# Kernel optimization log

Measured on AMD Instinct MI355X. Metric: run time of the kernel, lower is better.

Reference implementation:

```python
import jax, jax.numpy as jnp
import numpy as np

D_MODEL = 1024
NUM_HEADS = 16
D_K = D_MODEL // NUM_HEADS


def setup_inputs() -> dict:
    key = jax.random.key(0)
    ks = jax.random.split(key, 5)
    scale = 1.0 / np.sqrt(D_MODEL)
    x = jax.random.normal(ks[0], (4, 2048, D_MODEL), dtype=jnp.float32)
    W_qkv = jax.random.normal(ks[1], (D_MODEL, 3 * D_MODEL), dtype=jnp.float32) * scale
    b_qkv = jax.random.normal(ks[2], (3 * D_MODEL,), dtype=jnp.float32) * 0.02
    W_o = jax.random.normal(ks[3], (D_MODEL, D_MODEL), dtype=jnp.float32) * scale
    b_o = jax.random.normal(ks[4], (D_MODEL,), dtype=jnp.float32) * 0.02
    return {"x": x, "W_qkv": W_qkv, "b_qkv": b_qkv, "W_o": W_o, "b_o": b_o}


def reference(x, W_qkv, b_qkv, W_o, b_o):
    B, S, _ = x.shape
    qkv = x @ W_qkv + b_qkv  # [B, S, 3*D]
    q, k, v = jnp.split(qkv, 3, axis=-1)
    # [B, H, S, d_k]
    q = q.reshape(B, S, NUM_HEADS, D_K).transpose(0, 2, 1, 3)
    k = k.reshape(B, S, NUM_HEADS, D_K).transpose(0, 2, 1, 3)
    v = v.reshape(B, S, NUM_HEADS, D_K).transpose(0, 2, 1, 3)
    scores = jnp.einsum("bhqd,bhkd->bhqk", q, k) / jnp.sqrt(jnp.float32(D_K))
    causal = jnp.tril(jnp.ones((S, S), dtype=bool))  # [S, S]
    scores = jnp.where(causal[None, None], scores, jnp.float32(-1e9))
    attn = jax.nn.softmax(scores, axis=-1)
    out = jnp.einsum("bhqk,bhkd->bhqd", attn, v)  # [B, H, S, d_k]
    out = out.transpose(0, 2, 1, 3).reshape(B, S, D_MODEL)
    return out @ W_o + b_o
```

## Files before the change

### kernel.cpp

```cpp
#include <hip/hip_runtime.h>
#include <cstdint>
#include <cstddef>

typedef __bf16 bf16x8 __attribute__((ext_vector_type(8)));
typedef __bf16 bf16x4 __attribute__((ext_vector_type(4)));
typedef short s16x4 __attribute__((ext_vector_type(4)));
typedef float f32x4 __attribute__((ext_vector_type(4)));

__device__ __forceinline__ ushort f2bf(float f) {
  union { float f; uint32_t u; } v; v.f = f;
  uint32_t r = (v.u + 0x7fffu + ((v.u >> 16) & 1u)) >> 16;
  return (ushort)r;
}

__device__ __forceinline__ float fast_exp2(float x) {
#if defined(__HIP_DEVICE_COMPILE__) && __has_builtin(__builtin_amdgcn_exp2f)
  return __builtin_amdgcn_exp2f(x);
#else
  return exp2f(x);
#endif
}

__device__ __forceinline__ f32x4 mfma16(bf16x4 a, bf16x4 b, f32x4 c) {
#if defined(__HIP_DEVICE_COMPILE__)
#if __has_builtin(__builtin_amdgcn_mfma_f32_16x16x16_bf16)
  return __builtin_amdgcn_mfma_f32_16x16x16_bf16(a, b, c, 0, 0, 0);
#else
  return __builtin_amdgcn_mfma_f32_16x16x16bf16_1k(
      __builtin_bit_cast(s16x4, a), __builtin_bit_cast(s16x4, b), c, 0, 0, 0);
#endif
#else
  (void)a; (void)b;
  return c;
#endif
}

__device__ __forceinline__ void glds16(const ushort* g, ushort* l) {
  __builtin_amdgcn_global_load_lds((const __attribute__((address_space(1))) void*)g,
                                   (__attribute__((address_space(3))) void*)l, 16, 0, 0);
}

__global__ void conv_bf16(const float4* __restrict__ in, ushort4* __restrict__ out, int n4) {
  int i = blockIdx.x * blockDim.x + threadIdx.x;
  if (i < n4) {
    float4 v = in[i];
    ushort4 o;
    o.x = f2bf(v.x); o.y = f2bf(v.y); o.z = f2bf(v.z); o.w = f2bf(v.w);
    out[i] = o;
  }
}

__global__ void transpose_f32_bf16(const float* __restrict__ in, ushort* __restrict__ out,
                                   int R, int C) {
  __shared__ ushort t[32][33];
  int c0 = blockIdx.x * 32, r0 = blockIdx.y * 32;
  int tx = threadIdx.x, ty = threadIdx.y;
#pragma unroll
  for (int i = 0; i < 4; ++i)
    t[ty + i * 8][tx] = f2bf(in[(size_t)(r0 + ty + i * 8) * C + c0 + tx]);
  __syncthreads();
#pragma unroll
  for (int i = 0; i < 4; ++i)
    out[(size_t)(c0 + ty + i * 8) * R + r0 + tx] = t[tx][ty + i * 8];
}

template <int MODE>
__launch_bounds__(256)
__global__ void gemm_bt(const ushort* __restrict__ A, const ushort* __restrict__ Bt,
                        const float* __restrict__ bias,
                        ushort* __restrict__ o0, ushort* __restrict__ o1,
                        ushort* __restrict__ o2, float* __restrict__ of,
                        int M, int N, int K) {
  __shared__ ushort As[128 * 32];
  __shared__ ushort Bs[128 * 32];
  __shared__ ushort Ts[MODE == 0 ? 4 * 64 * 68 : 4];
  const int tid = threadIdx.x;
  const int wid = tid >> 6;
  const int lane = tid & 63;
  const int quad = lane >> 4;
  const int l16 = lane & 15;
  const int m0 = blockIdx.y * 128;
  const int n0 = blockIdx.x * 128;
  const int wm = (wid >> 1) * 64;
  const int wn = (wid & 1) * 64;
  const int srow = lane >> 2;
  const int scol = (lane & 3) << 3;

  f32x4 acc[4][4];
#pragma unroll
  for (int i = 0; i < 4; ++i)
#pragma unroll
    for (int j = 0; j < 4; ++j) acc[i][j] = (f32x4){0.f, 0.f, 0.f, 0.f};

  const int c0 = wid * 2, c1 = wid * 2 + 1;
  const ushort* gA0 = A + (size_t)(m0 + c0 * 16 + srow) * K + scol;
  const ushort* gA1 = A + (size_t)(m0 + c1 * 16 + srow) * K + scol;
  const ushort* gB0 = Bt + (size_t)(n0 + c0 * 16 + srow) * K + scol;
  const ushort* gB1 = Bt + (size_t)(n0 + c1 * 16 + srow) * K + scol;
  ushort* lA0 = As + c0 * 512 + lane * 8;
  ushort* lA1 = As + c1 * 512 + lane * 8;
  ushort* lB0 = Bs + c0 * 512 + lane * 8;
  ushort* lB1 = Bs + c1 * 512 + lane * 8;

  for (int k0 = 0; k0 < K; k0 += 32) {
    __syncthreads();
    glds16(gA0 + k0, lA0);
    glds16(gA1 + k0, lA1);
    glds16(gB0 + k0, lB0);
    glds16(gB1 + k0, lB1);
    __syncthreads();
    bf16x8 af[4], bfr[4];
#pragma unroll
    for (int i = 0; i < 4; ++i)
      af[i] = *(const bf16x8*)(As + (wm + i * 16 + l16) * 32 + quad * 8);
#pragma unroll
    for (int j = 0; j < 4; ++j)
      bfr[j] = *(const bf16x8*)(Bs + (wn + j * 16 + l16) * 32 + quad * 8);
#pragma unroll
    for (int i = 0; i < 4; ++i)
#pragma unroll
      for (int j = 0; j < 4; ++j)
        acc[i][j] = __builtin_amdgcn_mfma_f32_16x16x32_bf16(af[i], bfr[j], acc[i][j], 0, 0, 0);
  }

  if (MODE == 1) {
#pragma unroll
    for (int i = 0; i < 4; ++i)
#pragma unroll
      for (int j = 0; j < 4; ++j) {
        const int col = n0 + wn + j * 16 + l16;
        const float bv = bias[col];
#pragma unroll
        for (int r = 0; r < 4; ++r) {
          const int row = m0 + wm + i * 16 + quad * 4 + r;
          of[(size_t)row * N + col] = acc[i][j][r] + bv;
        }
      }
  } else {
    ushort* T = &Ts[wid * (64 * 68)];
    const int col0 = n0 + wn;
    const int sel = col0 >> 10;
    const int hh = (col0 & 1023) >> 6;
    const int row0 = m0 + wm;
    const int bb = row0 >> 11;
    const int s0 = row0 & 2047;
    const size_t bh = (size_t)(bb * 16 + hh);
#pragma unroll
    for (int j = 0; j < 4; ++j) {
      const float bv = bias[col0 + j * 16 + l16];
      const int dl = j * 16 + l16;
#pragma unroll
      for (int i = 0; i < 4; ++i) {
#pragma unroll
        for (int r = 0; r < 4; ++r) {
          const int sl = i * 16 + quad * 4 + r;
          float v = acc[i][j][r] + bv;
          if (sel == 0) v *= 0.18033688011112042f;
          const ushort u = f2bf(v);
          if (sel == 2) T[dl * 68 + sl] = u;
          else          T[sl * 68 + dl] = u;
        }
      }
    }
    asm volatile("s_waitcnt lgkmcnt(0)" ::: "memory");
    ushort* dst;
    if (sel == 2) dst = o2 + ((bh * 32 + (s0 >> 6)) << 12) + lane * 64;
    else          dst = (sel == 0 ? o0 : o1) + (bh * 2048 + s0 + lane) * 64;
    const ushort* Trow = &T[lane * 68];
#pragma unroll
    for (int k = 0; k < 16; ++k)
      *(ushort4*)(dst + k * 4) = *(const ushort4*)(Trow + k * 4);
  }
}

__launch_bounds__(256)
__global__ void attn_fused(const ushort* __restrict__ Qb, const ushort* __restrict__ Kb,
                           const ushort* __restrict__ Vt, ushort* __restrict__ Ob) {
  const int bh = blockIdx.y;
  const int pair = blockIdx.x;
  const int tid = threadIdx.x;
  const int wid = tid >> 6;
  const int lane = tid & 63;
  const int quad = lane >> 4;
  const int l16 = lane & 15;

  __shared__ ushort Ks[2][2][64 * 32];
  __shared__ ushort Vs[2][2][64 * 32];

  const int lr = lane >> 2;
  const int jphys = lane & 3;
  const int skey = (lr >> 1) & 3;
  const int jlog = jphys ^ skey;
  const int srow = wid * 16 + lr;
  const ushort* KgL = Kb + (size_t)bh * 2048 * 64 + (size_t)srow * 64 + jlog * 8;
  const ushort* VgL = Vt + (size_t)bh * 32 * 4096 + (size_t)srow * 64 + jlog * 8;
  ushort* ldsK0[2], *ldsK1[2], *ldsV0[2], *ldsV1[2];
#pragma unroll
  for (int buf = 0; buf < 2; ++buf) {
    ldsK0[buf] = &Ks[buf][0][wid * 16 * 32] + lane * 8;
    ldsK1[buf] = &Ks[buf][1][wid * 16 * 32] + lane * 8;
    ldsV0[buf] = &Vs[buf][0][wid * 16 * 32] + lane * 8;
    ldsV1[buf] = &Vs[buf][1][wid * 16 * 32] + lane * 8;
  }
  auto stage = [&](int jt) {
    const int buf = jt & 1;
    const ushort* ks = KgL + (size_t)jt * 4096;
    const ushort* vs = VgL + (size_t)jt * 4096;
    glds16(ks, ldsK0[buf]);
    glds16(ks + 32, ldsK1[buf]);
    glds16(vs, ldsV0[buf]);
    glds16(vs + 32, ldsV1[buf]);
  };

  const int rkey = (l16 >> 1) & 3;
  const int b = bh >> 4, h = bh & 15;

  auto process = [&](int qt) {
    const int qg0 = qt * 128 + wid * 32;

    const ushort* Qg = Qb + ((size_t)bh * 2048 + qg0) * 64;
    bf16x8 qa[2][2];
#pragma unroll
    for (int f = 0; f < 2; ++f)
#pragma unroll
      for (int hh = 0; hh < 2; ++hh)
        qa[f][hh] = *(const bf16x8*)(Qg + (f * 16 + l16) * 64 + hh * 32 + quad * 8);

    f32x4 o[2][4];
    float rs[2];
#pragma unroll
    for (int f = 0; f < 2; ++f) {
      rs[f] = 0.f;
#pragma unroll
      for (int m = 0; m < 4; ++m) o[f][m] = (f32x4){0.f, 0.f, 0.f, 0.f};
    }

    const int nIt = 2 * qt + 2;
    stage(0);

    for (int jt = 0; jt < nIt; ++jt) {
      __syncthreads();
      if (jt + 1 < nIt) stage(jt + 1);

      const int kvb = jt * 64;
      if (kvb > qg0 + 31) continue;
      const int buf = jt & 1;

      f32x4 s[2][4];
#pragma unroll
      for (int n = 0; n < 4; ++n) {
        const int koff = (n * 16 + l16) * 32 + (quad ^ rkey) * 8;
        bf16x8 kb0 = *(const bf16x8*)&Ks[buf][0][koff];
        bf16x8 kb1 = *(const bf16x8*)&Ks[buf][1][koff];
#pragma unroll
        for (int f = 0; f < 2; ++f) {
          f32x4 z = (f32x4){0.f, 0.f, 0.f, 0.f};
          z = __builtin_amdgcn_mfma_f32_16x16x32_bf16(kb0, qa[f][0], z, 0, 0, 0);
          z = __builtin_amdgcn_mfma_f32_16x16x32_bf16(kb1, qa[f][1], z, 0, 0, 0);
          s[f][n] = z;
        }
      }

      bf16x4 p[2][4];
      if (kvb + 63 <= qg0) {
#pragma unroll
        for (int f = 0; f < 2; ++f)
#pragma unroll
          for (int n = 0; n < 4; ++n) {
            float pe[4];
#pragma unroll
            for (int r = 0; r < 4; ++r) {
              pe[r] = fast_exp2(s[f][n][r]);
              rs[f] += pe[r];
            }
            p[f][n] = (bf16x4){(__bf16)pe[0], (__bf16)pe[1], (__bf16)pe[2], (__bf16)pe[3]};
          }
      } else {
#pragma unroll
        for (int f = 0; f < 2; ++f) {
          const int qg = qg0 + f * 16 + l16;
#pragma unroll
          for (int n = 0; n < 4; ++n) {
            const int kg0 = kvb + n * 16 + quad * 4;
            float pe[4];
#pragma unroll
            for (int r = 0; r < 4; ++r) {
              float e = fast_exp2(s[f][n][r]);
              pe[r] = (kg0 + r > qg) ? 0.f : e;
              rs[f] += pe[r];
            }
            p[f][n] = (bf16x4){(__bf16)pe[0], (__bf16)pe[1], (__bf16)pe[2], (__bf16)pe[3]};
          }
        }
      }

#pragma unroll
      for (int m = 0; m < 4; ++m) {
        const int vrow = (m * 16 + l16) * 32;
#pragma unroll
        for (int n = 0; n < 4; ++n) {
          const int clog = (n & 1) * 2 + (quad >> 1);
          const int voff = vrow + (clog ^ rkey) * 8 + (quad & 1) * 4;
          bf16x4 va = *(const bf16x4*)&Vs[buf][n >> 1][voff];
#pragma unroll
          for (int f = 0; f < 2; ++f) o[f][m] = mfma16(va, p[f][n], o[f][m]);
        }
      }
    }

#pragma unroll
    for (int f = 0; f < 2; ++f) {
      float t = rs[f];
      t += __shfl_xor(t, 16, 64);
      t += __shfl_xor(t, 32, 64);
      const float il = 1.f / t;
      const int q = qg0 + f * 16 + l16;
      ushort* dst = Ob + ((size_t)b * 2048 + q) * 1024 + h * 64;
#pragma unroll
      for (int m = 0; m < 4; ++m) {
        ushort4 w;
        w.x = f2bf(o[f][m][0] * il);
        w.y = f2bf(o[f][m][1] * il);
        w.z = f2bf(o[f][m][2] * il);
        w.w = f2bf(o[f][m][3] * il);
        *(ushort4*)(dst + m * 16 + quad * 4) = w;
      }
    }
  };

  process(15 - pair);
  __syncthreads();
  process(pair);
}

extern "C" void kernel_launch(void* const* d_in, const int* in_sizes, int n_in,
                              void* d_out, int out_size, void* d_ws, size_t ws_size,
                              hipStream_t stream) {
  const float* x    = (const float*)d_in[0];
  const float* Wqkv = (const float*)d_in[1];
  const float* bqkv = (const float*)d_in[2];
  const float* Wo   = (const float*)d_in[3];
  const float* bo   = (const float*)d_in[4];
  float* out = (float*)d_out;

  char* ws = (char*)d_ws;
  size_t off = 0;
  auto alloc = [&](size_t bytes) {
    void* p = ws + off;
    off += (bytes + 255) & ~(size_t)255;
    return p;
  };
  ushort* xbf    = (ushort*)alloc((size_t)8192 * 1024 * 2);
  ushort* Wqkv_t = (ushort*)alloc((size_t)3072 * 1024 * 2);
  ushort* Wo_t   = (ushort*)alloc((size_t)1024 * 1024 * 2);
  ushort* Qb     = (ushort*)alloc((size_t)64 * 2048 * 64 * 2);
  ushort* Kb     = (ushort*)alloc((size_t)64 * 2048 * 64 * 2);
  ushort* Vb     = (ushort*)alloc((size_t)64 * 2048 * 64 * 2);
  ushort* Ab     = (ushort*)alloc((size_t)8192 * 1024 * 2);

  conv_bf16<<<dim3(8192), dim3(256), 0, stream>>>((const float4*)x, (ushort4*)xbf,
                                                  8192 * 1024 / 4);
  transpose_f32_bf16<<<dim3(96, 32), dim3(32, 8), 0, stream>>>(Wqkv, Wqkv_t, 1024, 3072);
  transpose_f32_bf16<<<dim3(32, 32), dim3(32, 8), 0, stream>>>(Wo, Wo_t, 1024, 1024);
  gemm_bt<0><<<dim3(24, 64), dim3(256), 0, stream>>>(xbf, Wqkv_t, bqkv, Qb, Kb, Vb, nullptr,
                                                     8192, 3072, 1024);
  attn_fused<<<dim3(8, 64), dim3(256), 0, stream>>>(Qb, Kb, Vb, Ab);
  gemm_bt<1><<<dim3(8, 64), dim3(256), 0, stream>>>(Ab, Wo_t, bo, nullptr, nullptr, nullptr,
                                                    out, 8192, 1024, 1024);
}
```

Before: 273.5 us.

## Replace QKV GEMM with 256x256-tile 8-wave pipelined kernel using direct global-to-LDS loads

Adds a new QKV projection GEMM that uses 256x256 output tiles with 512 threads. It double-buffers global-to-LDS loads, uses an XOR-swizzled shared layout, and interleaves quarter-tile MFMA phases with explicit barriers and waitcnts. Workgroup IDs are remapped for L2 locality, and the epilogue writes Q/K/V (with V in a transposed tile layout) through LDS for coalesced stores. The goal is higher data reuse and better latency hiding than the 128-tile GEMM it replaces. In exchange it carries heavy register and LDS pressure and relies on fragile hand-tuned synchronization.

Measured after the change: 274.6 us. No clear change (+0.4%).

```diff
diff --git a/kernel.cpp b/kernel.cpp
--- a/kernel.cpp
+++ b/kernel.cpp
@@ -62,6 +62,203 @@
 #pragma unroll
   for (int i = 0; i < 4; ++i)
     out[(size_t)(c0 + ty + i * 8) * R + r0 + tx] = t[tx][ty + i * 8];
+}
+
+#define BAR8() do { asm volatile("" ::: "memory"); \
+                    __builtin_amdgcn_s_barrier();  \
+                    asm volatile("" ::: "memory"); } while (0)
+#define LGKM0() asm volatile("s_waitcnt lgkmcnt(0)" ::: "memory")
+#define VMC6()  asm volatile("s_waitcnt vmcnt(6)" ::: "memory")
+#define VMC4()  asm volatile("s_waitcnt vmcnt(4)" ::: "memory")
+#define VMC0()  asm volatile("s_waitcnt vmcnt(0)" ::: "memory")
+
+#define LOADA(b_, qm_) do {                                               \
+    const ushort* _ab = smem + ((b_) * 2 + (qm_)) * 8192 + aRow;          \
+    _Pragma("unroll")                                                     \
+    for (int m_ = 0; m_ < 4; ++m_) {                                      \
+      aF[m_][0] = *(const bf16x8*)(_ab + m_ * 1024 + cK0);                \
+      aF[m_][1] = *(const bf16x8*)(_ab + m_ * 1024 + cK1);                \
+    }                                                                     \
+  } while (0)
+
+#define LOADB(b_, qn_) do {                                               \
+    const ushort* _bb = smem + 32768 + ((b_) * 2 + (qn_)) * 8192 + bRow;  \
+    _Pragma("unroll")                                                     \
+    for (int n_ = 0; n_ < 2; ++n_) {                                      \
+      bF[qn_][n_][0] = *(const bf16x8*)(_bb + n_ * 1024 + cK0);           \
+      bF[qn_][n_][1] = *(const bf16x8*)(_bb + n_ * 1024 + cK1);           \
+    }                                                                     \
+  } while (0)
+
+#define MMAC(qm_, qn_) do {                                               \
+    __builtin_amdgcn_s_setprio(1);                                        \
+    _Pragma("unroll")                                                     \
+    for (int m_ = 0; m_ < 4; ++m_)                                        \
+      _Pragma("unroll")                                                   \
+      for (int n_ = 0; n_ < 2; ++n_) {                                    \
+        acc[(qm_) * 4 + m_][(qn_) * 2 + n_] =                             \
+            __builtin_amdgcn_mfma_f32_16x16x32_bf16(                      \
+                aF[m_][0], bF[qn_][n_][0],                                \
+                acc[(qm_) * 4 + m_][(qn_) * 2 + n_], 0, 0, 0);            \
+        acc[(qm_) * 4 + m_][(qn_) * 2 + n_] =                             \
+            __builtin_amdgcn_mfma_f32_16x16x32_bf16(                      \
+                aF[m_][1], bF[qn_][n_][1],                                \
+                acc[(qm_) * 4 + m_][(qn_) * 2 + n_], 0, 0, 0);            \
+      }                                                                   \
+    __builtin_amdgcn_s_setprio(0);                                        \
+  } while (0)
+
+__launch_bounds__(512, 2)
+__global__ void gemm8_qkv(const ushort* __restrict__ A, const ushort* __restrict__ Bt,
+                          const float* __restrict__ bias,
+                          ushort* __restrict__ o0, ushort* __restrict__ o1,
+                          ushort* __restrict__ o2) {
+  constexpr int K = 1024;
+  constexpr int NT = 16;
+  __shared__ ushort smem[65536];
+
+  const int tid = threadIdx.x;
+  const int wid = tid >> 6;
+  const int lane = tid & 63;
+  const int quad = lane >> 4;
+  const int l16 = lane & 15;
+  const int wr = wid >> 2;
+  const int wc = wid & 3;
+
+  int wg = blockIdx.y * gridDim.x + blockIdx.x;
+  const int nwgx = gridDim.x;
+  const int cpx = (nwgx * gridDim.y) >> 3;
+  wg = (wg & 7) * cpx + (wg >> 3);
+  const int m0 = (wg / nwgx) * 256;
+  const int n0 = (wg % nwgx) * 256;
+
+  const int r0 = tid >> 3;
+  const int cch = (tid & 7) ^ (r0 & 7);
+  const ushort* gA = A + (size_t)(m0 + r0) * K + cch * 8;
+  const ushort* gB = Bt + (size_t)(n0 + r0) * K + cch * 8;
+  ushort* lA = smem + tid * 8;
+  ushort* lB = smem + 32768 + tid * 8;
+
+  auto stageA = [&](int t, int h, int b) {
+    const ushort* s = gA + (h * 128) * K + t * 64;
+    ushort* d = lA + (b * 2 + h) * 8192;
+    glds16(s, d);
+    glds16(s + 64 * K, d + 4096);
+  };
+  auto stageB = [&](int t, int h, int b) {
+    const ushort* s = gB + (h * 128) * K + t * 64;
+    ushort* d = lB + (b * 2 + h) * 8192;
+    glds16(s, d);
+    glds16(s + 64 * K, d + 4096);
+  };
+
+  const int rkey = l16 & 7;
+  const int aRow = (wr * 64 + l16) * 64;
+  const int bRow = (wc * 32 + l16) * 64;
+  const int cK0 = (quad ^ rkey) * 8;
+  const int cK1 = ((quad + 4) ^ rkey) * 8;
+
+  f32x4 acc[8][4];
+#pragma unroll
+  for (int i = 0; i < 8; ++i)
+#pragma unroll
+    for (int j = 0; j < 4; ++j) acc[i][j] = (f32x4){0.f, 0.f, 0.f, 0.f};
+  bf16x8 aF[4][2], bF[2][2][2];
+
+  stageA(0, 0, 0); stageB(0, 0, 0); stageA(0, 1, 0); stageB(0, 1, 0);
+  VMC4();
+  stageA(1, 0, 1); stageB(1, 0, 1); stageB(1, 1, 1);
+  VMC6();
+  BAR8();
+
+#pragma unroll 2
+  for (int t = 0; t < NT; ++t) {
+    const int b = t & 1;
+    LOADA(b, 0);
+    LOADB(b, 0);
+    if (t + 1 < NT) stageA(t + 1, 1, b ^ 1);
+    BAR8();
+    LGKM0();
+    MMAC(0, 0);
+    BAR8();
+    LOADB(b, 1);
+    if (t + 2 < NT) stageA(t + 2, 0, b);
+    BAR8();
+    LGKM0();
+    MMAC(0, 1);
+    BAR8();
+    LOADA(b, 1);
+    if (t + 2 < NT) stageB(t + 2, 0, b);
+    BAR8();
+    LGKM0();
+    MMAC(1, 0);
+    BAR8();
+    if (t + 2 < NT) stageB(t + 2, 1, b);
+    BAR8();
+    LGKM0();
+    MMAC(1, 1);
+    if (t == NT - 2) { VMC0(); } else if (t < NT - 2) { VMC6(); }
+    BAR8();
+  }
+
+  const int colr = n0 & 1023;
+  const int sel = n0 >> 10;
+  const int hbase = colr >> 6;
+  const int bb = m0 >> 11;
+  const int s0 = m0 & 2047;
+
+#pragma unroll
+  for (int m = 0; m < 8; ++m) {
+    const int Rl = (m >> 2) * 128 + wr * 64 + (m & 3) * 16 + quad * 4;
+#pragma unroll
+    for (int n = 0; n < 4; ++n) {
+      const int C = (n >> 1) * 128 + wc * 32 + (n & 1) * 16 + l16;
+      const float bv = bias[n0 + C];
+#pragma unroll
+      for (int r = 0; r < 4; ++r) {
+        float v = acc[m][n][r] + bv;
+        if (sel == 0) v *= 0.18033688011112042f;
+        const ushort u = f2bf(v);
+        const int R = Rl + r;
+        if (sel == 2)
+          smem[(C << 8) + ((((R >> 3) ^ (C & 7)) << 3) | (R & 7))] = u;
+        else
+          smem[(R << 8) + ((((C >> 3) ^ (R & 7)) << 3) | (C & 7))] = u;
+      }
+    }
+  }
+  __syncthreads();
+
+  if (sel != 2) {
+    ushort* o = sel ? o1 : o0;
+#pragma unroll
+    for (int l = 0; l < 2; ++l) {
+      const int q = l * 512 + tid;
+      const int hh = q >> 8;
+      const int s_loc = q & 255;
+      ushort* dst = o + ((size_t)((bb * 16 + hbase + hh) * 2048 + s0 + s_loc)) * 64;
+      const int key = s_loc & 7;
+      const uint4* srow = (const uint4*)(smem + (s_loc << 8));
+#pragma unroll
+      for (int g = 0; g < 8; ++g)
+        ((uint4*)dst)[g] = srow[(hh * 8 + g) ^ key];
+    }
+  } else {
+#pragma unroll
+    for (int l = 0; l < 2; ++l) {
+      const int q = l * 512 + tid;
+      const int sc4 = q >> 8;
+      const int d_loc = q & 255;
+      ushort* dst = o2 +
+          ((size_t)((bb * 16 + hbase + (d_loc >> 6)) * 32 + (s0 >> 6) + sc4) << 12) +
+          (d_loc & 63) * 64;
+      const int key = d_loc & 7;
+      const uint4* srow = (const uint4*)(smem + (d_loc << 8));
+#pragma unroll
+      for (int g = 0; g < 8; ++g)
+        ((uint4*)dst)[g] = srow[(sc4 * 8 + g) ^ key];
+    }
+  }
 }
 
 template <int MODE>
@@ -362,8 +559,7 @@
                                                   8192 * 1024 / 4);
   transpose_f32_bf16<<<dim3(96, 32), dim3(32, 8), 0, stream>>>(Wqkv, Wqkv_t, 1024, 3072);
   transpose_f32_bf16<<<dim3(32, 32), dim3(32, 8), 0, stream>>>(Wo, Wo_t, 1024, 1024);
-  gemm_bt<0><<<dim3(24, 64), dim3(256), 0, stream>>>(xbf, Wqkv_t, bqkv, Qb, Kb, Vb, nullptr,
-                                                     8192, 3072, 1024);
+  gemm8_qkv<<<dim3(12, 32), dim3(512), 0, stream>>>(xbf, Wqkv_t, bqkv, Qb, Kb, Vb);
   attn_fused<<<dim3(8, 64), dim3(256), 0, stream>>>(Qb, Kb, Vb, Ab);
   gemm_bt<1><<<dim3(8, 64), dim3(256), 0, stream>>>(Ab, Wo_t, bo, nullptr, nullptr, nullptr,
                                                     out, 8192, 1024, 1024);
```

## Replace QKV GEMM with 256x192-tile kernel using direct-to-LDS loads and swizzled epilogue

Applied to the files above, without the earlier changes.

Adds a dedicated QKV projection kernel that computes 256x192 output tiles with 8x6 MFMA 16x16x32 accumulators per wave and double-buffered global-to-LDS staging. Workgroups are remapped for L2 locality, and the MFMA bursts run at raised wave priority. The epilogue scales Q and writes Q/K/V head-major through a swizzled LDS transpose, with V in a blocked layout. The aim is higher arithmetic intensity and fewer LDS round trips than the 128x128 generic GEMM, at the cost of heavy register pressure and many barriers per K-step.

Result: slower. 297.4 us (+8.7%).

```diff
diff --git a/kernel.cpp b/kernel.cpp
--- a/kernel.cpp
+++ b/kernel.cpp
@@ -62,6 +62,171 @@
 #pragma unroll
   for (int i = 0; i < 4; ++i)
     out[(size_t)(c0 + ty + i * 8) * R + r0 + tx] = t[tx][ty + i * 8];
+}
+
+#define BAR8() do { asm volatile("" ::: "memory"); \
+                    __builtin_amdgcn_s_barrier();  \
+                    asm volatile("" ::: "memory"); } while (0)
+#define VMC0()  asm volatile("s_waitcnt vmcnt(0)" ::: "memory")
+
+__launch_bounds__(256, 2)
+__global__ void gemm8_qkv(const ushort* __restrict__ A, const ushort* __restrict__ Bt,
+                          const float* __restrict__ bias,
+                          ushort* __restrict__ o0, ushort* __restrict__ o1,
+                          ushort* __restrict__ o2) {
+  constexpr int K = 1024;
+  constexpr int NT = 32;
+  __shared__ ushort smem[28672];
+
+  const int tid = threadIdx.x;
+  const int wid = tid >> 6;
+  const int lane = tid & 63;
+  const int quad = lane >> 4;
+  const int l16 = lane & 15;
+  const int wr = wid >> 1;
+  const int wc = wid & 1;
+
+  int wg = blockIdx.y * gridDim.x + blockIdx.x;
+  wg = (wg & 7) * 64 + (wg >> 3);
+  const int m0 = (wg >> 4) * 256;
+  const int n0 = (wg & 15) * 192;
+
+  const int r_l = lane >> 2;
+  const int q_l = ((lane & 3) - (r_l >> 1)) & 3;
+  const ushort* gA0 = A + (size_t)(m0 + wid * 64 + r_l) * K + q_l * 8;
+  const ushort* gB0 = Bt + (size_t)(n0 + wid * 48 + r_l) * K + q_l * 8;
+  ushort* dA0 = smem + wid * 2048 + lane * 8;
+  ushort* dB0 = smem + 16384 + wid * 1536 + lane * 8;
+
+  auto stageAll = [&](int t1, int bs) {
+    const ushort* sa = gA0 + t1 * 32;
+    ushort* da = dA0 + bs * 8192;
+#pragma unroll
+    for (int u = 0; u < 4; ++u) glds16(sa + u * 16 * K, da + u * 512);
+    const ushort* sb = gB0 + t1 * 32;
+    ushort* db = dB0 + bs * 6144;
+#pragma unroll
+    for (int u = 0; u < 3; ++u) glds16(sb + u * 16 * K, db + u * 512);
+  };
+
+  const int slot8 = (l16 * 4 + ((quad + (l16 >> 1)) & 3)) * 8;
+
+  f32x4 acc[8][6];
+#pragma unroll
+  for (int i = 0; i < 8; ++i)
+#pragma unroll
+    for (int j = 0; j < 6; ++j) acc[i][j] = (f32x4){0.f, 0.f, 0.f, 0.f};
+  bf16x8 aFr[2], bFr[6];
+
+  auto loadB6 = [&](int b) {
+#pragma unroll
+    for (int n = 0; n < 6; ++n)
+      bFr[n] = *(const bf16x8*)(smem + 16384 + b * 6144 + (wc * 6 + n) * 512 + slot8);
+  };
+  auto loadA2 = [&](int b, int mp) {
+#pragma unroll
+    for (int m = 0; m < 2; ++m)
+      aFr[m] = *(const bf16x8*)(smem + b * 8192 + (wr * 8 + mp * 2 + m) * 512 + slot8);
+  };
+  auto mma12 = [&](int mp) {
+    __builtin_amdgcn_s_setprio(1);
+#pragma unroll
+    for (int m = 0; m < 2; ++m)
+#pragma unroll
+      for (int n = 0; n < 6; ++n)
+        acc[mp * 2 + m][n] = __builtin_amdgcn_mfma_f32_16x16x32_bf16(
+            aFr[m], bFr[n], acc[mp * 2 + m][n], 0, 0, 0);
+    __builtin_amdgcn_s_setprio(0);
+  };
+
+  stageAll(0, 0);
+  VMC0();
+  BAR8();
+
+#pragma unroll 2
+  for (int t = 0; t < NT; ++t) {
+    const int b = t & 1;
+    loadB6(b);
+    loadA2(b, 0);
+    if (t + 1 < NT) stageAll(t + 1, b ^ 1);
+    BAR8();
+    mma12(0);
+    BAR8();
+    loadA2(b, 1);
+    BAR8();
+    mma12(1);
+    BAR8();
+    loadA2(b, 2);
+    BAR8();
+    mma12(2);
+    BAR8();
+    loadA2(b, 3);
+    BAR8();
+    mma12(3);
+    if (t + 1 < NT) VMC0();
+    BAR8();
+  }
+
+  const int bb = m0 >> 11;
+  const int s0 = m0 & 2047;
+
+#pragma unroll
+  for (int hc = 0; hc < 3; ++hc) {
+    const int gc0 = n0 + hc * 64;
+    const int sel = gc0 >> 10;
+    const int head = (gc0 & 1023) >> 6;
+    const size_t bh = (size_t)(bb * 16 + head);
+    if (hc) __syncthreads();
+#pragma unroll
+    for (int j = 0; j < 6; ++j) {
+      const int cf = wc * 6 + j;
+      if ((cf >> 2) == hc) {
+        const int dloc = cf * 16 + l16 - hc * 64;
+        const float bv = bias[gc0 + dloc];
+#pragma unroll
+        for (int i = 0; i < 8; ++i) {
+#pragma unroll
+          for (int r = 0; r < 4; ++r) {
+            const int R = wr * 128 + i * 16 + quad * 4 + r;
+            float v = acc[i][j][r] + bv;
+            if (sel == 0) v *= 0.18033688011112042f;
+            const ushort u = f2bf(v);
+            if (sel == 2) {
+              const int lc = R >> 3;
+              const int key = ((dloc & 1) << 2) | (lc >> 3);
+              const int phys = (lc & 24) | ((lc ^ key) & 7);
+              smem[dloc * 256 + phys * 8 + (R & 7)] = u;
+            } else {
+              smem[R * 64 + (((dloc >> 3) ^ (R & 7)) << 3) + (dloc & 7)] = u;
+            }
+          }
+        }
+      }
+    }
+    __syncthreads();
+    if (sel != 2) {
+      ushort* o = sel ? o1 : o0;
+      const int R = tid;
+      ushort* dst = o + (bh * 2048 + s0 + R) * 64;
+      const int key = R & 7;
+      const uint4* srow = (const uint4*)(smem + R * 64);
+#pragma unroll
+      for (int g = 0; g < 8; ++g)
+        ((uint4*)dst)[g] = srow[g ^ key];
+    } else {
+      const int d = tid >> 2;
+      const int sq = tid & 3;
+      ushort* dst = o2 + (((size_t)(bh * 32 + (s0 >> 6) + sq)) << 12) + d * 64;
+      const uint4* srow = (const uint4*)(smem + d * 256);
+#pragma unroll
+      for (int g = 0; g < 8; ++g) {
+        const int lc = sq * 8 + g;
+        const int key = ((d & 1) << 2) | sq;
+        const int phys = (lc & 24) | ((lc ^ key) & 7);
+        ((uint4*)dst)[g] = srow[phys];
+      }
+    }
+  }
 }
 
 template <int MODE>
@@ -362,8 +527,7 @@
                                                   8192 * 1024 / 4);
   transpose_f32_bf16<<<dim3(96, 32), dim3(32, 8), 0, stream>>>(Wqkv, Wqkv_t, 1024, 3072);
   transpose_f32_bf16<<<dim3(32, 32), dim3(32, 8), 0, stream>>>(Wo, Wo_t, 1024, 1024);
-  gemm_bt<0><<<dim3(24, 64), dim3(256), 0, stream>>>(xbf, Wqkv_t, bqkv, Qb, Kb, Vb, nullptr,
-                                                     8192, 3072, 1024);
+  gemm8_qkv<<<dim3(16, 32), dim3(256), 0, stream>>>(xbf, Wqkv_t, bqkv, Qb, Kb, Vb);
   attn_fused<<<dim3(8, 64), dim3(256), 0, stream>>>(Qb, Kb, Vb, Ab);
   gemm_bt<1><<<dim3(8, 64), dim3(256), 0, stream>>>(Ab, Wo_t, bo, nullptr, nullptr, nullptr,
                                                     out, 8192, 1024, 1024);
```

## Triple-buffer GEMM LDS pipeline, swizzle tiles, remap workgroups for XCD locality

Applied to the files above, without the earlier changes.

Rewrites the GEMM main loop to keep three LDS stages in flight, prefetching two tiles ahead. It uses partial vmcnt waits and a single barrier per iteration in place of two __syncthreads per k-step, and swizzles LDS slots to avoid bank conflicts. Workgroup ids in both the GEMM and attention kernels are remapped so neighbouring tiles land on the same XCD for L2 reuse. s_setprio is raised around the MFMA blocks. The QKV epilogue now stages through the shared buffer with XOR swizzling and 16-byte stores, at the cost of extra barriers and tighter occupancy assumptions via launch_bounds(256,3).

Measured after the change: 259.7 us. -5.1%, faster.

```diff
diff --git a/kernel.cpp b/kernel.cpp
--- a/kernel.cpp
+++ b/kernel.cpp
@@ -64,27 +64,57 @@
     out[(size_t)(c0 + ty + i * 8) * R + r0 + tx] = t[tx][ty + i * 8];
 }
 
+#define BAR8() do { asm volatile("" ::: "memory"); \
+                    __builtin_amdgcn_s_barrier();  \
+                    asm volatile("" ::: "memory"); } while (0)
+#define VMC4()  asm volatile("s_waitcnt vmcnt(4)" ::: "memory")
+#define VMC0()  asm volatile("s_waitcnt vmcnt(0)" ::: "memory")
+
 template <int MODE>
-__launch_bounds__(256)
-__global__ void gemm_bt(const ushort* __restrict__ A, const ushort* __restrict__ Bt,
+__launch_bounds__(256, 3)
+__global__ void gemm_tb(const ushort* __restrict__ A, const ushort* __restrict__ Bt,
                         const float* __restrict__ bias,
                         ushort* __restrict__ o0, ushort* __restrict__ o1,
                         ushort* __restrict__ o2, float* __restrict__ of,
                         int M, int N, int K) {
-  __shared__ ushort As[128 * 32];
-  __shared__ ushort Bs[128 * 32];
-  __shared__ ushort Ts[MODE == 0 ? 4 * 64 * 68 : 4];
+  __shared__ ushort smem[24576];
+  const int NT = K >> 5;
   const int tid = threadIdx.x;
   const int wid = tid >> 6;
   const int lane = tid & 63;
   const int quad = lane >> 4;
   const int l16 = lane & 15;
-  const int m0 = blockIdx.y * 128;
-  const int n0 = blockIdx.x * 128;
   const int wm = (wid >> 1) * 64;
   const int wn = (wid & 1) * 64;
-  const int srow = lane >> 2;
-  const int scol = (lane & 3) << 3;
+
+  int wg = blockIdx.y * gridDim.x + blockIdx.x;
+  const int ntx = gridDim.x;
+  const int cpx = (ntx * gridDim.y) >> 3;
+  wg = (wg & 7) * cpx + (wg >> 3);
+  const int m0 = (wg / ntx) * 128;
+  const int n0 = (wg % ntx) * 128;
+
+  const int r_l = lane >> 2;
+  const int q_l = ((lane & 3) - (r_l >> 1)) & 3;
+  const ushort* gA0 = A + (size_t)(m0 + wid * 32 + r_l) * K + q_l * 8;
+  const ushort* gB0 = Bt + (size_t)(n0 + wid * 32 + r_l) * K + q_l * 8;
+  ushort* dA0 = smem + wid * 1024 + lane * 8;
+  ushort* dB0 = smem + 12288 + wid * 1024 + lane * 8;
+
+  auto stage = [&](int t, int bs) {
+    const ushort* sa = gA0 + t * 32;
+    ushort* da = dA0 + bs * 4096;
+    glds16(sa, da);
+    glds16(sa + 16 * K, da + 512);
+    const ushort* sb = gB0 + t * 32;
+    ushort* db = dB0 + bs * 4096;
+    glds16(sb, db);
+    glds16(sb + 16 * K, db + 512);
+  };
+
+  const int slot8 = (l16 * 4 + ((quad + (l16 >> 1)) & 3)) * 8;
+  const int abase = (wm >> 4) * 512 + slot8;
+  const int bbase = 12288 + (wn >> 4) * 512 + slot8;
 
   f32x4 acc[4][4];
 #pragma unroll
@@ -92,35 +122,33 @@
 #pragma unroll
     for (int j = 0; j < 4; ++j) acc[i][j] = (f32x4){0.f, 0.f, 0.f, 0.f};
 
-  const int c0 = wid * 2, c1 = wid * 2 + 1;
-  const ushort* gA0 = A + (size_t)(m0 + c0 * 16 + srow) * K + scol;
-  const ushort* gA1 = A + (size_t)(m0 + c1 * 16 + srow) * K + scol;
-  const ushort* gB0 = Bt + (size_t)(n0 + c0 * 16 + srow) * K + scol;
-  const ushort* gB1 = Bt + (size_t)(n0 + c1 * 16 + srow) * K + scol;
-  ushort* lA0 = As + c0 * 512 + lane * 8;
-  ushort* lA1 = As + c1 * 512 + lane * 8;
-  ushort* lB0 = Bs + c0 * 512 + lane * 8;
-  ushort* lB1 = Bs + c1 * 512 + lane * 8;
-
-  for (int k0 = 0; k0 < K; k0 += 32) {
-    __syncthreads();
-    glds16(gA0 + k0, lA0);
-    glds16(gA1 + k0, lA1);
-    glds16(gB0 + k0, lB0);
-    glds16(gB1 + k0, lB1);
-    __syncthreads();
+  stage(0, 0);
+  stage(1, 1);
+  VMC4();
+  BAR8();
+
+  int b = 0;
+  for (int t = 0; t < NT; ++t) {
     bf16x8 af[4], bfr[4];
+    const int boff = b * 4096;
 #pragma unroll
     for (int i = 0; i < 4; ++i)
-      af[i] = *(const bf16x8*)(As + (wm + i * 16 + l16) * 32 + quad * 8);
+      af[i] = *(const bf16x8*)(smem + boff + abase + i * 512);
 #pragma unroll
     for (int j = 0; j < 4; ++j)
-      bfr[j] = *(const bf16x8*)(Bs + (wn + j * 16 + l16) * 32 + quad * 8);
+      bfr[j] = *(const bf16x8*)(smem + boff + bbase + j * 512);
+    const int b2 = (b == 0) ? 2 : b - 1;
+    if (t + 2 < NT) stage(t + 2, b2);
+    __builtin_amdgcn_s_setprio(1);
 #pragma unroll
     for (int i = 0; i < 4; ++i)
 #pragma unroll
       for (int j = 0; j < 4; ++j)
         acc[i][j] = __builtin_amdgcn_mfma_f32_16x16x32_bf16(af[i], bfr[j], acc[i][j], 0, 0, 0);
+    __builtin_amdgcn_s_setprio(0);
+    if (t + 2 < NT) { VMC4(); } else if (t + 1 < NT) { VMC0(); }
+    BAR8();
+    b = (b == 2) ? 0 : b + 1;
   }
 
   if (MODE == 1) {
@@ -137,47 +165,72 @@
         }
       }
   } else {
-    ushort* T = &Ts[wid * (64 * 68)];
-    const int col0 = n0 + wn;
-    const int sel = col0 >> 10;
-    const int hh = (col0 & 1023) >> 6;
-    const int row0 = m0 + wm;
-    const int bb = row0 >> 11;
-    const int s0 = row0 & 2047;
-    const size_t bh = (size_t)(bb * 16 + hh);
-#pragma unroll
-    for (int j = 0; j < 4; ++j) {
-      const float bv = bias[col0 + j * 16 + l16];
-      const int dl = j * 16 + l16;
-#pragma unroll
-      for (int i = 0; i < 4; ++i) {
-#pragma unroll
-        for (int r = 0; r < 4; ++r) {
-          const int sl = i * 16 + quad * 4 + r;
-          float v = acc[i][j][r] + bv;
-          if (sel == 0) v *= 0.18033688011112042f;
-          const ushort u = f2bf(v);
-          if (sel == 2) T[dl * 68 + sl] = u;
-          else          T[sl * 68 + dl] = u;
+    const int bb = m0 >> 11;
+    const int s0 = m0 & 2047;
+    const int wr = wid >> 1;
+    const int wcol = wid & 1;
+#pragma unroll
+    for (int hc = 0; hc < 2; ++hc) {
+      const int gc0 = n0 + hc * 64;
+      const int sel = gc0 >> 10;
+      const int head = (gc0 & 1023) >> 6;
+      const size_t bh = (size_t)(bb * 16 + head);
+      __syncthreads();
+      if (wcol == hc) {
+#pragma unroll
+        for (int j = 0; j < 4; ++j) {
+          const int dloc = j * 16 + l16;
+          const float bv = bias[gc0 + dloc];
+#pragma unroll
+          for (int i = 0; i < 4; ++i) {
+#pragma unroll
+            for (int r = 0; r < 4; ++r) {
+              const int R = wr * 64 + i * 16 + quad * 4 + r;
+              float v = acc[i][j][r] + bv;
+              if (sel == 0) v *= 0.18033688011112042f;
+              const ushort u = f2bf(v);
+              if (sel == 2) {
+                const int lc = R >> 3;
+                smem[dloc * 128 + ((lc ^ (dloc & 7)) << 3) + (R & 7)] = u;
+              } else {
+                smem[R * 64 + (((dloc >> 3) ^ (R & 7)) << 3) + (dloc & 7)] = u;
+              }
+            }
+          }
         }
       }
+      __syncthreads();
+      if (sel != 2) {
+        ushort* o = sel ? o1 : o0;
+        const int R = tid >> 1;
+        const int gh = tid & 1;
+        ushort* dst = o + (bh * 2048 + s0 + R) * 64 + gh * 32;
+        const int key = R & 7;
+        const uint4* srow = (const uint4*)(smem + R * 64);
+#pragma unroll
+        for (int g = 0; g < 4; ++g)
+          ((uint4*)dst)[g] = srow[(gh * 4 + g) ^ key];
+      } else {
+        const int d = tid >> 2;
+        const int sq = tid & 3;
+        ushort* dst = o2 + (((size_t)(bh * 32 + (s0 >> 6) + (sq >> 1))) << 12) +
+                      d * 64 + (sq & 1) * 32;
+        const uint4* srow = (const uint4*)(smem + d * 128);
+#pragma unroll
+        for (int g = 0; g < 4; ++g)
+          ((uint4*)dst)[g] = srow[(sq * 4 + g) ^ (d & 7)];
+      }
     }
-    asm volatile("s_waitcnt lgkmcnt(0)" ::: "memory");
-    ushort* dst;
-    if (sel == 2) dst = o2 + ((bh * 32 + (s0 >> 6)) << 12) + lane * 64;
-    else          dst = (sel == 0 ? o0 : o1) + (bh * 2048 + s0 + lane) * 64;
-    const ushort* Trow = &T[lane * 68];
-#pragma unroll
-    for (int k = 0; k < 16; ++k)
-      *(ushort4*)(dst + k * 4) = *(const ushort4*)(Trow + k * 4);
   }
 }
 
 __launch_bounds__(256)
 __global__ void attn_fused(const ushort* __restrict__ Qb, const ushort* __restrict__ Kb,
                            const ushort* __restrict__ Vt, ushort* __restrict__ Ob) {
-  const int bh = blockIdx.y;
-  const int pair = blockIdx.x;
+  int wg0 = blockIdx.y * 8 + blockIdx.x;
+  const int w = (wg0 & 7) * 64 + (wg0 >> 3);
+  const int bh = w >> 3;
+  const int pair = w & 7;
   const int tid = threadIdx.x;
   const int wid = tid >> 6;
   const int lane = tid & 63;
@@ -247,6 +300,7 @@
       const int buf = jt & 1;
 
       f32x4 s[2][4];
+      __builtin_amdgcn_s_setprio(1);
 #pragma unroll
       for (int n = 0; n < 4; ++n) {
         const int koff = (n * 16 + l16) * 32 + (quad ^ rkey) * 8;
@@ -260,6 +314,7 @@
           s[f][n] = z;
         }
       }
+      __builtin_amdgcn_s_setprio(0);
 
       bf16x4 p[2][4];
       if (kvb + 63 <= qg0) {
@@ -294,6 +349,7 @@
         }
       }
 
+      __builtin_amdgcn_s_setprio(1);
 #pragma unroll
       for (int m = 0; m < 4; ++m) {
         const int vrow = (m * 16 + l16) * 32;
@@ -306,6 +362,7 @@
           for (int f = 0; f < 2; ++f) o[f][m] = mfma16(va, p[f][n], o[f][m]);
         }
       }
+      __builtin_amdgcn_s_setprio(0);
     }
 
 #pragma unroll
@@ -318,12 +375,12 @@
       ushort* dst = Ob + ((size_t)b * 2048 + q) * 1024 + h * 64;
 #pragma unroll
       for (int m = 0; m < 4; ++m) {
-        ushort4 w;
-        w.x = f2bf(o[f][m][0] * il);
-        w.y = f2bf(o[f][m][1] * il);
-        w.z = f2bf(o[f][m][2] * il);
-        w.w = f2bf(o[f][m][3] * il);
-        *(ushort4*)(dst + m * 16 + quad * 4) = w;
+        ushort4 w2;
+        w2.x = f2bf(o[f][m][0] * il);
+        w2.y = f2bf(o[f][m][1] * il);
+        w2.z = f2bf(o[f][m][2] * il);
+        w2.w = f2bf(o[f][m][3] * il);
+        *(ushort4*)(dst + m * 16 + quad * 4) = w2;
       }
     }
   };
@@ -362,9 +419,9 @@
                                                   8192 * 1024 / 4);
   transpose_f32_bf16<<<dim3(96, 32), dim3(32, 8), 0, stream>>>(Wqkv, Wqkv_t, 1024, 3072);
   transpose_f32_bf16<<<dim3(32, 32), dim3(32, 8), 0, stream>>>(Wo, Wo_t, 1024, 1024);
-  gemm_bt<0><<<dim3(24, 64), dim3(256), 0, stream>>>(xbf, Wqkv_t, bqkv, Qb, Kb, Vb, nullptr,
+  gemm_tb<0><<<dim3(24, 64), dim3(256), 0, stream>>>(xbf, Wqkv_t, bqkv, Qb, Kb, Vb, nullptr,
                                                      8192, 3072, 1024);
   attn_fused<<<dim3(8, 64), dim3(256), 0, stream>>>(Qb, Kb, Vb, Ab);
-  gemm_bt<1><<<dim3(8, 64), dim3(256), 0, stream>>>(Ab, Wo_t, bo, nullptr, nullptr, nullptr,
+  gemm_tb<1><<<dim3(8, 64), dim3(256), 0, stream>>>(Ab, Wo_t, bo, nullptr, nullptr, nullptr,
                                                     out, 8192, 1024, 1024);
 }
```
